# Kernel tuning notes

Measured on AMD Instinct MI355X. Metric: run time of the kernel, lower is better.

## Reference

```python
import jax, jax.numpy as jnp
import numpy as np

B, T, D, H = 8, 512, 1024, 16
DH = D // H  # per-head feature dim (64)


def setup_inputs() -> dict:
    key = jax.random.key(0)
    ks = jax.random.split(key, 10)
    s = 1.0 / np.sqrt(DH)
    inp = {
        "X_data": jax.random.normal(ks[0], (B, T, D), dtype=jnp.float32),
        "mask": jnp.ones((B, T), dtype=jnp.int32),
        # per-head Q/K/V projections (each SelfAttention has its own d_h x d_h weights)
        "Wq": jax.random.normal(ks[1], (H, DH, DH), dtype=jnp.float32) * s,
        "bq": jnp.zeros((H, DH), dtype=jnp.float32),
        "Wk": jax.random.normal(ks[2], (H, DH, DH), dtype=jnp.float32) * s,
        "bk": jnp.zeros((H, DH), dtype=jnp.float32),
        "Wv": jax.random.normal(ks[3], (H, DH, DH), dtype=jnp.float32) * s,
        "bv": jnp.zeros((H, DH), dtype=jnp.float32),
        # AttentionFusion: linear on concatenated head outputs -> len_feature_new
        "Wf": jax.random.normal(ks[4], (D, D), dtype=jnp.float32) * (1.0 / np.sqrt(D)),
        "bf": jnp.zeros((D,), dtype=jnp.float32),
    }
    return inp


def reference(X_data, mask, Wq, bq, Wk, bk, Wv, bv, Wf, bf):
    # Split features into heads: [B, T, H, DH] (equal partitions since D % H == 0)
    Xh = X_data.reshape(B, T, H, DH)
    # Batched per-head projections (replaces the Python loop over heads)
    Q = jnp.einsum("bthd,hde->bhte", Xh, Wq) + bq[None, :, None, :]
    K = jnp.einsum("bthd,hde->bhte", Xh, Wk) + bk[None, :, None, :]
    V = jnp.einsum("bthd,hde->bhte", Xh, Wv) + bv[None, :, None, :]
    scale = 1.0 / jnp.sqrt(jnp.asarray(DH, dtype=Q.dtype))
    scores = jnp.einsum("bhqe,bhke->bhqk", Q, K) * scale  # [B, H, T, T]
    scores = jnp.where(mask[:, None, None, :] > 0, scores, jnp.asarray(-1e9, scores.dtype))
    att = jax.nn.softmax(scores, axis=-1)
    out = jnp.einsum("bhqk,bhke->bhqe", att, V)  # [B, H, T, DH]
    # Concatenate heads (same order as the per-head loop) and fuse
    out = out.transpose(0, 2, 1, 3).reshape(B, T, D)
    fused = out @ Wf + bf  # AttentionFusion linear
    return fused
```

## Files before the change

kernel.cpp:

```cpp
#include <hip/hip_runtime.h>
#include <math.h>

#define B 8
#define T 512
#define D 1024
#define H 16
#define DH 64

typedef __bf16 bf16;
typedef __attribute__((ext_vector_type(8))) __bf16 bf16x8;
typedef __attribute__((ext_vector_type(4))) float f32x4;

__device__ __forceinline__ void gld16(const void* g, void* l) {
    __builtin_amdgcn_global_load_lds(
        (const __attribute__((address_space(1))) void*)g,
        (__attribute__((address_space(3))) void*)l, 16, 0, 0);
}


#define EXP2SCALE 1.44269504088896f

__global__ __launch_bounds__(256) void prep_w(
    const float* __restrict__ Wq, const float* __restrict__ Wk,
    const float* __restrict__ Wv, const float* __restrict__ Wf,
    bf16* __restrict__ WqT, bf16* __restrict__ WkT,
    bf16* __restrict__ WvT, bf16* __restrict__ WfT)
{
    __shared__ bf16 Ts[64 * 72];
    const int blk = blockIdx.x, tid = threadIdx.x;
    if (blk < 48) {
        const int m = blk >> 4, h = blk & 15;
        const float* src = (m == 0 ? Wq : (m == 1 ? Wk : Wv)) + h * 4096;
        bf16* dst = (m == 0 ? WqT : (m == 1 ? WkT : WvT)) + h * 4096;
        for (int i = tid; i < 1024; i += 256) {
            const int d = i >> 4, eq = (i & 15) * 4;
            const float4 w = *(const float4*)(src + d * 64 + eq);
            Ts[(eq + 0) * 72 + d] = (bf16)w.x; Ts[(eq + 1) * 72 + d] = (bf16)w.y;
            Ts[(eq + 2) * 72 + d] = (bf16)w.z; Ts[(eq + 3) * 72 + d] = (bf16)w.w;
        }
        __syncthreads();
        for (int i = tid; i < 512; i += 256) {
            const int e = i >> 3, kc = (i & 7) * 8;
            *(bf16x8*)(dst + e * 64 + kc) = *(const bf16x8*)&Ts[e * 72 + kc];
        }
    } else {
        const int ti = blk - 48, k0 = (ti >> 4) * 64, n0 = (ti & 15) * 64;
        for (int i = tid; i < 1024; i += 256) {
            const int k = i >> 4, nq = (i & 15) * 4;
            const float4 w = *(const float4*)(Wf + (size_t)(k0 + k) * D + n0 + nq);
            Ts[(nq + 0) * 72 + k] = (bf16)w.x; Ts[(nq + 1) * 72 + k] = (bf16)w.y;
            Ts[(nq + 2) * 72 + k] = (bf16)w.z; Ts[(nq + 3) * 72 + k] = (bf16)w.w;
        }
        __syncthreads();
        for (int i = tid; i < 512; i += 256) {
            const int n = i >> 3, kc = (i & 7) * 8;
            *(bf16x8*)(WfT + (size_t)(n0 + n) * D + k0 + kc) = *(const bf16x8*)&Ts[n * 72 + kc];
        }
    }
}

__global__ __launch_bounds__(256, 2) void qkv_attn(
    const float* __restrict__ X, const int* __restrict__ mask,
    const bf16* __restrict__ WqT, const bf16* __restrict__ WkT,
    const bf16* __restrict__ WvT,
    const float* __restrict__ bq, const float* __restrict__ bk,
    const float* __restrict__ bv,
    bf16* __restrict__ Ob)
{
    __shared__ __align__(16) char smem[80384];
    bf16* Wks = (bf16*)(smem);
    bf16* Wvs = (bf16*)(smem + 8192);
    bf16* Pl  = (bf16*)(smem + 53248);
    bf16* Xkt = (bf16*)(smem + 71680);
    int*  msk = (int*)(smem + 79872);
    bf16* Wqs   = (bf16*)(smem + 16384);
    bf16* Xq    = Pl;
    bf16* Stage = Pl;
    bf16* Ostage = Pl;

    const int bh = blockIdx.x & 127, q0 = (blockIdx.x >> 7) * 128;
    const int b = bh >> 4, h = bh & 15;
    const int tid = threadIdx.x, wave = tid >> 6, lane = tid & 63;
    const int quad = lane >> 4, l15 = lane & 15;
    const int lr = lane >> 3, lc = lane & 7;
    const int csw = (lc ^ lr) * 8;

    const int pkrow = wave * 16 + (lane >> 2);
    const int pc0 = (lane & 3) * 2;

    float bqr[4], bkr[4], bvr[4];
#pragma unroll
    for (int nt = 0; nt < 4; ++nt) {
        bqr[nt] = bq[h * DH + nt * 16 + l15];
        bkr[nt] = bk[h * DH + nt * 16 + l15];
        bvr[nt] = bv[h * DH + nt * 16 + l15];
    }

    float4 px0, px1, px2, px3;
    {
        const float* src = X + (size_t)(b * T + pkrow) * D + h * DH + pc0 * 8;
        px0 = *(const float4*)src; px1 = *(const float4*)(src + 4);
        px2 = *(const float4*)(src + 8); px3 = *(const float4*)(src + 12);
    }
    int mreg = (tid < 64) ? mask[(size_t)b * T + tid] : 0;

    {
        const int r1 = wave * 16;
#pragma unroll
        for (int j = 0; j < 2; ++j) {
            gld16(WqT + (size_t)h * 4096 + (r1 + j * 8 + lr) * 64 + csw, &Wqs[(r1 + j * 8) * 64]);
            gld16(WkT + (size_t)h * 4096 + (r1 + j * 8 + lr) * 64 + csw, &Wks[(r1 + j * 8) * 64]);
            gld16(WvT + (size_t)h * 4096 + (r1 + j * 8 + lr) * 64 + csw, &Wvs[(r1 + j * 8) * 64]);
        }
    }
    for (int i = tid; i < 1024; i += 256) {
        const int row = i >> 3, c = i & 7;
        const float* src = X + (size_t)(b * T + q0 + row) * D + h * DH + c * 8;
        const float4 x0 = *(const float4*)src;
        const float4 x1 = *(const float4*)(src + 4);
        bf16x8 t;
        t[0] = (bf16)x0.x; t[1] = (bf16)x0.y; t[2] = (bf16)x0.z; t[3] = (bf16)x0.w;
        t[4] = (bf16)x1.x; t[5] = (bf16)x1.y; t[6] = (bf16)x1.z; t[7] = (bf16)x1.w;
        *(bf16x8*)&Xq[row * 64 + ((c ^ (row & 7)) * 8)] = t;
    }
    __syncthreads();

    {
        f32x4 accQ[2][4] = {};
#pragma unroll
        for (int ks = 0; ks < 2; ++ks) {
            bf16x8 af[2], bfr[4];
#pragma unroll
            for (int mt = 0; mt < 2; ++mt) {
                const int row = wave * 32 + mt * 16 + l15;
                af[mt] = *(const bf16x8*)&Xq[row * 64 + (((ks * 4 + quad) ^ (l15 & 7)) * 8)];
            }
#pragma unroll
            for (int nt = 0; nt < 4; ++nt)
                bfr[nt] = *(const bf16x8*)&Wqs[(nt * 16 + l15) * 64 + (((ks * 4 + quad) ^ (l15 & 7)) * 8)];
#pragma unroll
            for (int mt = 0; mt < 2; ++mt)
#pragma unroll
                for (int nt = 0; nt < 4; ++nt)
                    accQ[mt][nt] = __builtin_amdgcn_mfma_f32_16x16x32_bf16(af[mt], bfr[nt], accQ[mt][nt], 0, 0, 0);
        }
        __syncthreads();
        const float qs = 0.125f * EXP2SCALE;
#pragma unroll
        for (int mt = 0; mt < 2; ++mt)
#pragma unroll
            for (int nt = 0; nt < 4; ++nt)
#pragma unroll
                for (int reg = 0; reg < 4; ++reg)
                    Stage[(wave * 32 + mt * 16 + quad * 4 + reg) * 72 + nt * 16 + l15] =
                        (bf16)((accQ[mt][nt][reg] + bqr[nt]) * qs);
        __builtin_amdgcn_wave_barrier();
    }
    bf16x8 qf[2][2];
#pragma unroll
    for (int mt = 0; mt < 2; ++mt)
#pragma unroll
        for (int ks = 0; ks < 2; ++ks)
            qf[mt][ks] = *(const bf16x8*)&Stage[(wave * 32 + mt * 16 + l15) * 72 + ks * 32 + quad * 8];

    f32x4 acc[2][4] = {};
    float lst[2][4] = {};

    for (int kt = 0; kt < 8; ++kt) {
        const int p = kt & 1;
        bf16* Ks  = (bf16*)(smem + 16384 + p * 9216);
        bf16* Vts = (bf16*)(smem + 34816 + p * 9216);

        {
            bf16x8 t0, t1;
            t0[0] = (bf16)px0.x; t0[1] = (bf16)px0.y; t0[2] = (bf16)px0.z; t0[3] = (bf16)px0.w;
            t0[4] = (bf16)px1.x; t0[5] = (bf16)px1.y; t0[6] = (bf16)px1.z; t0[7] = (bf16)px1.w;
            t1[0] = (bf16)px2.x; t1[1] = (bf16)px2.y; t1[2] = (bf16)px2.z; t1[3] = (bf16)px2.w;
            t1[4] = (bf16)px3.x; t1[5] = (bf16)px3.y; t1[6] = (bf16)px3.z; t1[7] = (bf16)px3.w;
            *(bf16x8*)&Xkt[pkrow * 64 + ((pc0 ^ (pkrow & 7)) * 8)] = t0;
            *(bf16x8*)&Xkt[pkrow * 64 + (((pc0 + 1) ^ (pkrow & 7)) * 8)] = t1;
            if (tid < 64) msk[p * 64 + tid] = mreg;
        }
        __builtin_amdgcn_wave_barrier();

        if (kt < 7) {
            const float* src = X + (size_t)(b * T + (kt + 1) * 64 + pkrow) * D + h * DH + pc0 * 8;
            px0 = *(const float4*)src; px1 = *(const float4*)(src + 4);
            px2 = *(const float4*)(src + 8); px3 = *(const float4*)(src + 12);
            if (tid < 64) mreg = mask[(size_t)b * T + (kt + 1) * 64 + tid];
        }

        {
            bf16x8 afkv[2];
#pragma unroll
            for (int ks = 0; ks < 2; ++ks)
                afkv[ks] = *(const bf16x8*)&Xkt[(wave * 16 + l15) * 64 + (((ks * 4 + quad) ^ (l15 & 7)) * 8)];
            f32x4 accK[4] = {}, accV[4] = {};
#pragma unroll
            for (int ks = 0; ks < 2; ++ks)
#pragma unroll
                for (int nt = 0; nt < 4; ++nt) {
                    const bf16x8 bk8 = *(const bf16x8*)&Wks[(nt * 16 + l15) * 64 + (((ks * 4 + quad) ^ (l15 & 7)) * 8)];
                    accK[nt] = __builtin_amdgcn_mfma_f32_16x16x32_bf16(afkv[ks], bk8, accK[nt], 0, 0, 0);
                    const bf16x8 bv8 = *(const bf16x8*)&Wvs[(nt * 16 + l15) * 64 + (((ks * 4 + quad) ^ (l15 & 7)) * 8)];
                    accV[nt] = __builtin_amdgcn_mfma_f32_16x16x32_bf16(afkv[ks], bv8, accV[nt], 0, 0, 0);
                }
#pragma unroll
            for (int nt = 0; nt < 4; ++nt)
#pragma unroll
                for (int reg = 0; reg < 4; ++reg) {
                    const int key = wave * 16 + quad * 4 + reg;
                    const int e = nt * 16 + l15;
                    Ks[key * 72 + e] = (bf16)(accK[nt][reg] + bkr[nt]);
                    Vts[e * 72 + key] = (bf16)(accV[nt][reg] + bvr[nt]);
                }
        }
        __syncthreads();

        bf16* Plw = Pl + wave * (32 * 72);
        {
            bf16x8 kf[4][2];
#pragma unroll
            for (int nt = 0; nt < 4; ++nt)
#pragma unroll
                for (int ks = 0; ks < 2; ++ks)
                    kf[nt][ks] = *(const bf16x8*)&Ks[(nt * 16 + l15) * 72 + ks * 32 + quad * 8];
            int mv[4];
#pragma unroll
            for (int nt = 0; nt < 4; ++nt) mv[nt] = msk[p * 64 + nt * 16 + l15];
#pragma unroll
            for (int mt = 0; mt < 2; ++mt) {
                f32x4 s[4] = {};
#pragma unroll
                for (int ks = 0; ks < 2; ++ks)
#pragma unroll
                    for (int nt = 0; nt < 4; ++nt)
                        s[nt] = __builtin_amdgcn_mfma_f32_16x16x32_bf16(qf[mt][ks], kf[nt][ks], s[nt], 0, 0, 0);
#pragma unroll
                for (int nt = 0; nt < 4; ++nt)
#pragma unroll
                    for (int reg = 0; reg < 4; ++reg) {
                        const float pv = (mv[nt] > 0) ? exp2f(s[nt][reg]) : 0.f;
                        lst[mt][reg] += pv;
                        Plw[(mt * 16 + quad * 4 + reg) * 72 + nt * 16 + l15] = (bf16)pv;
                    }
            }
        }
        __builtin_amdgcn_wave_barrier();

#pragma unroll
        for (int kc = 0; kc < 2; ++kc) {
            const bf16x8 pf0 = *(const bf16x8*)&Plw[(l15) * 72 + kc * 32 + quad * 8];
            const bf16x8 pf1 = *(const bf16x8*)&Plw[(16 + l15) * 72 + kc * 32 + quad * 8];
#pragma unroll
            for (int nt = 0; nt < 4; ++nt) {
                const bf16x8 vf = *(const bf16x8*)&Vts[(nt * 16 + l15) * 72 + kc * 32 + quad * 8];
                acc[0][nt] = __builtin_amdgcn_mfma_f32_16x16x32_bf16(pf0, vf, acc[0][nt], 0, 0, 0);
                acc[1][nt] = __builtin_amdgcn_mfma_f32_16x16x32_bf16(pf1, vf, acc[1][nt], 0, 0, 0);
            }
        }
    }

    __builtin_amdgcn_wave_barrier();
#pragma unroll
    for (int mt = 0; mt < 2; ++mt)
#pragma unroll
        for (int reg = 0; reg < 4; ++reg) {
            float l = lst[mt][reg];
            l += __shfl_xor(l, 1);
            l += __shfl_xor(l, 2);
            l += __shfl_xor(l, 4);
            l += __shfl_xor(l, 8);
            const float inv = 1.f / l;
            const int row = wave * 32 + mt * 16 + quad * 4 + reg;
#pragma unroll
            for (int nt = 0; nt < 4; ++nt)
                Ostage[row * 72 + nt * 16 + l15] = (bf16)(acc[mt][nt][reg] * inv);
        }
    __syncthreads();
    for (int i = tid; i < 1024; i += 256) {
        const int row = i >> 3, c = (i & 7) * 8;
        *(bf16x8*)(Ob + ((size_t)b * T + q0 + row) * D + h * DH + c) =
            *(const bf16x8*)&Ostage[row * 72 + c];
    }
}

__global__ __launch_bounds__(256, 2) void fuse_mfma(
    const bf16* __restrict__ Ob, const bf16* __restrict__ WfT,
    const float* __restrict__ bfv, float* __restrict__ out)
{
    __shared__ __align__(16) char smem[49152];

    const int col0 = blockIdx.x * 64;
    const int row0 = blockIdx.y * 128;
    const int tid = threadIdx.x, wave = tid >> 6, lane = tid & 63;
    const int quad = lane >> 4, l15 = lane & 15;
    const int lr = lane >> 3, lc = lane & 7;
    const int wm = wave * 32;

    f32x4 acc[2][4] = {};

    auto stage = [&](int k0, int buf) {
        bf16* As = (bf16*)(smem + buf * 16384);
        bf16* Bs = (bf16*)(smem + 32768 + buf * 8192);
#pragma unroll
        for (int j = 0; j < 4; ++j) {
            const int row = wm + j * 8 + lr;
            gld16(Ob + (size_t)(row0 + row) * D + k0 + ((lc ^ (row & 7)) * 8),
                  &As[(wm + j * 8) * 64]);
        }
#pragma unroll
        for (int j = 0; j < 2; ++j) {
            const int row = wave * 16 + j * 8 + lr;
            gld16(WfT + (size_t)(col0 + row) * D + k0 + ((lc ^ (row & 7)) * 8),
                  &Bs[(wave * 16 + j * 8) * 64]);
        }
    };

    stage(0, 0);
    __syncthreads();

    for (int i = 0; i < 16; ++i) {
        const int buf = i & 1;
        if (i < 15) stage((i + 1) * 64, buf ^ 1);
        bf16* As = (bf16*)(smem + buf * 16384);
        bf16* Bs = (bf16*)(smem + 32768 + buf * 8192);
#pragma unroll
        for (int ks = 0; ks < 2; ++ks) {
            bf16x8 af[2], bfr[4];
#pragma unroll
            for (int mt = 0; mt < 2; ++mt) {
                const int row = wm + mt * 16 + l15;
                af[mt] = *(const bf16x8*)&As[row * 64 + (((ks * 4 + quad) ^ (l15 & 7)) * 8)];
            }
#pragma unroll
            for (int nt = 0; nt < 4; ++nt)
                bfr[nt] = *(const bf16x8*)&Bs[(nt * 16 + l15) * 64 + (((ks * 4 + quad) ^ (l15 & 7)) * 8)];
#pragma unroll
            for (int mt = 0; mt < 2; ++mt)
#pragma unroll
                for (int nt = 0; nt < 4; ++nt)
                    acc[mt][nt] = __builtin_amdgcn_mfma_f32_16x16x32_bf16(af[mt], bfr[nt], acc[mt][nt], 0, 0, 0);
        }
        __syncthreads();
    }

    float* Ofs = (float*)smem;
    float bias[4];
#pragma unroll
    for (int nt = 0; nt < 4; ++nt) bias[nt] = bfv[col0 + nt * 16 + l15];
#pragma unroll
    for (int mt = 0; mt < 2; ++mt)
#pragma unroll
        for (int reg = 0; reg < 4; ++reg) {
            const int row = wm + mt * 16 + quad * 4 + reg;
#pragma unroll
            for (int nt = 0; nt < 4; ++nt)
                Ofs[row * 68 + nt * 16 + l15] = acc[mt][nt][reg] + bias[nt];
        }
    __syncthreads();
    for (int i = tid; i < 2048; i += 256) {
        const int row = i >> 4, c = (i & 15) * 4;
        *(float4*)(out + (size_t)(row0 + row) * D + col0 + c) = *(const float4*)&Ofs[row * 68 + c];
    }
}

extern "C" void kernel_launch(void* const* d_in, const int* in_sizes, int n_in,
                              void* d_out, int out_size, void* d_ws, size_t ws_size,
                              hipStream_t stream) {
    const float* X   = (const float*)d_in[0];
    const int* mask  = (const int*)d_in[1];
    const float* Wq  = (const float*)d_in[2];
    const float* bq  = (const float*)d_in[3];
    const float* Wk  = (const float*)d_in[4];
    const float* bk  = (const float*)d_in[5];
    const float* Wv  = (const float*)d_in[6];
    const float* bv  = (const float*)d_in[7];
    const float* Wf  = (const float*)d_in[8];
    const float* bfv = (const float*)d_in[9];
    float* out = (float*)d_out;

    bf16* wsb = (bf16*)d_ws;
    const size_t QN = (size_t)B * H * T * DH;
    bf16* Ob  = wsb;
    bf16* WfT = wsb + QN;
    bf16* WqT = WfT + (size_t)D * D;
    bf16* WkT = WqT + H * DH * DH;
    bf16* WvT = WkT + H * DH * DH;

    prep_w<<<dim3(304), 256, 0, stream>>>(Wq, Wk, Wv, Wf, WqT, WkT, WvT, WfT);
    qkv_attn<<<dim3(512), 256, 0, stream>>>(X, mask, WqT, WkT, WvT, bq, bk, bv, Ob);
    fuse_mfma<<<dim3(D / 64, (B * T) / 128), 256, 0, stream>>>(Ob, WfT, bfv, out);
}
```

Before: 130.7 us.

## Transpose MFMA operands for packed stores, fold biases, widen fusion GEMM tile

Measured after the change: 128.4 us. No clear change (-1.8%).

```diff
diff --git a/kernel.cpp b/kernel.cpp
--- a/kernel.cpp
+++ b/kernel.cpp
@@ -9,6 +9,7 @@
 
 typedef __bf16 bf16;
 typedef __attribute__((ext_vector_type(8))) __bf16 bf16x8;
+typedef __attribute__((ext_vector_type(4))) __bf16 bf16x4;
 typedef __attribute__((ext_vector_type(4))) float f32x4;
 
 __device__ __forceinline__ void gld16(const void* g, void* l) {
@@ -84,15 +85,15 @@
     const int quad = lane >> 4, l15 = lane & 15;
     const int lr = lane >> 3, lc = lane & 7;
     const int csw = (lc ^ lr) * 8;
+    (void)bk;
 
     const int pkrow = wave * 16 + (lane >> 2);
     const int pc0 = (lane & 3) * 2;
 
-    float bqr[4], bkr[4], bvr[4];
+    float bqr[4], bvr[4];
 #pragma unroll
     for (int nt = 0; nt < 4; ++nt) {
         bqr[nt] = bq[h * DH + nt * 16 + l15];
-        bkr[nt] = bk[h * DH + nt * 16 + l15];
         bvr[nt] = bv[h * DH + nt * 16 + l15];
     }
 
@@ -164,7 +165,7 @@
             qf[mt][ks] = *(const bf16x8*)&Stage[(wave * 32 + mt * 16 + l15) * 72 + ks * 32 + quad * 8];
 
     f32x4 acc[2][4] = {};
-    float lst[2][4] = {};
+    float lst2[2] = {0.f, 0.f};
 
     for (int kt = 0; kt < 8; ++kt) {
         const int p = kt & 1;
@@ -201,19 +202,21 @@
 #pragma unroll
                 for (int nt = 0; nt < 4; ++nt) {
                     const bf16x8 bk8 = *(const bf16x8*)&Wks[(nt * 16 + l15) * 64 + (((ks * 4 + quad) ^ (l15 & 7)) * 8)];
-                    accK[nt] = __builtin_amdgcn_mfma_f32_16x16x32_bf16(afkv[ks], bk8, accK[nt], 0, 0, 0);
+                    accK[nt] = __builtin_amdgcn_mfma_f32_16x16x32_bf16(bk8, afkv[ks], accK[nt], 0, 0, 0);
                     const bf16x8 bv8 = *(const bf16x8*)&Wvs[(nt * 16 + l15) * 64 + (((ks * 4 + quad) ^ (l15 & 7)) * 8)];
                     accV[nt] = __builtin_amdgcn_mfma_f32_16x16x32_bf16(afkv[ks], bv8, accV[nt], 0, 0, 0);
                 }
 #pragma unroll
-            for (int nt = 0; nt < 4; ++nt)
-#pragma unroll
-                for (int reg = 0; reg < 4; ++reg) {
-                    const int key = wave * 16 + quad * 4 + reg;
-                    const int e = nt * 16 + l15;
-                    Ks[key * 72 + e] = (bf16)(accK[nt][reg] + bkr[nt]);
-                    Vts[e * 72 + key] = (bf16)(accV[nt][reg] + bvr[nt]);
-                }
+            for (int nt = 0; nt < 4; ++nt) {
+                bf16x4 kp;
+#pragma unroll
+                for (int reg = 0; reg < 4; ++reg) kp[reg] = (bf16)accK[nt][reg];
+                *(bf16x4*)&Ks[(wave * 16 + l15) * 72 + nt * 16 + quad * 4] = kp;
+                bf16x4 vp;
+#pragma unroll
+                for (int reg = 0; reg < 4; ++reg) vp[reg] = (bf16)accV[nt][reg];
+                *(bf16x4*)&Vts[(nt * 16 + l15) * 72 + wave * 16 + quad * 4] = vp;
+            }
         }
         __syncthreads();
 
@@ -225,9 +228,10 @@
 #pragma unroll
                 for (int ks = 0; ks < 2; ++ks)
                     kf[nt][ks] = *(const bf16x8*)&Ks[(nt * 16 + l15) * 72 + ks * 32 + quad * 8];
-            int mv[4];
-#pragma unroll
-            for (int nt = 0; nt < 4; ++nt) mv[nt] = msk[p * 64 + nt * 16 + l15];
+            int4 mv4[4];
+#pragma unroll
+            for (int nt = 0; nt < 4; ++nt)
+                mv4[nt] = *(const int4*)&msk[p * 64 + nt * 16 + quad * 4];
 #pragma unroll
             for (int mt = 0; mt < 2; ++mt) {
                 f32x4 s[4] = {};
@@ -235,15 +239,18 @@
                 for (int ks = 0; ks < 2; ++ks)
 #pragma unroll
                     for (int nt = 0; nt < 4; ++nt)
-                        s[nt] = __builtin_amdgcn_mfma_f32_16x16x32_bf16(qf[mt][ks], kf[nt][ks], s[nt], 0, 0, 0);
-#pragma unroll
-                for (int nt = 0; nt < 4; ++nt)
-#pragma unroll
-                    for (int reg = 0; reg < 4; ++reg) {
-                        const float pv = (mv[nt] > 0) ? exp2f(s[nt][reg]) : 0.f;
-                        lst[mt][reg] += pv;
-                        Plw[(mt * 16 + quad * 4 + reg) * 72 + nt * 16 + l15] = (bf16)pv;
-                    }
+                        s[nt] = __builtin_amdgcn_mfma_f32_16x16x32_bf16(kf[nt][ks], qf[mt][ks], s[nt], 0, 0, 0);
+#pragma unroll
+                for (int nt = 0; nt < 4; ++nt) {
+                    bf16x4 pp;
+                    const float p0 = (mv4[nt].x > 0) ? exp2f(s[nt][0]) : 0.f;
+                    const float p1 = (mv4[nt].y > 0) ? exp2f(s[nt][1]) : 0.f;
+                    const float p2 = (mv4[nt].z > 0) ? exp2f(s[nt][2]) : 0.f;
+                    const float p3 = (mv4[nt].w > 0) ? exp2f(s[nt][3]) : 0.f;
+                    lst2[mt] += (p0 + p1) + (p2 + p3);
+                    pp[0] = (bf16)p0; pp[1] = (bf16)p1; pp[2] = (bf16)p2; pp[3] = (bf16)p3;
+                    *(bf16x4*)&Plw[(mt * 16 + l15) * 72 + nt * 16 + quad * 4] = pp;
+                }
             }
         }
         __builtin_amdgcn_wave_barrier();
@@ -262,20 +269,26 @@
     }
 
     __builtin_amdgcn_wave_barrier();
+    float inv_r[2][4];
+#pragma unroll
+    for (int mt = 0; mt < 2; ++mt) {
+        float l = lst2[mt];
+        l += __shfl_xor(l, 16);
+        l += __shfl_xor(l, 32);
+        const float inv = 1.f / l;
+#pragma unroll
+        for (int reg = 0; reg < 4; ++reg)
+            inv_r[mt][reg] = __shfl(inv, (lane & 48) | (quad * 4 + reg));
+    }
 #pragma unroll
     for (int mt = 0; mt < 2; ++mt)
 #pragma unroll
         for (int reg = 0; reg < 4; ++reg) {
-            float l = lst[mt][reg];
-            l += __shfl_xor(l, 1);
-            l += __shfl_xor(l, 2);
-            l += __shfl_xor(l, 4);
-            l += __shfl_xor(l, 8);
-            const float inv = 1.f / l;
             const int row = wave * 32 + mt * 16 + quad * 4 + reg;
 #pragma unroll
             for (int nt = 0; nt < 4; ++nt)
-                Ostage[row * 72 + nt * 16 + l15] = (bf16)(acc[mt][nt][reg] * inv);
+                Ostage[row * 72 + nt * 16 + l15] =
+                    (bf16)(acc[mt][nt][reg] * inv_r[mt][reg] + bvr[nt]);
         }
     __syncthreads();
     for (int i = tid; i < 1024; i += 256) {
@@ -289,31 +302,27 @@
     const bf16* __restrict__ Ob, const bf16* __restrict__ WfT,
     const float* __restrict__ bfv, float* __restrict__ out)
 {
-    __shared__ __align__(16) char smem[49152];
-
-    const int col0 = blockIdx.x * 64;
+    __shared__ __align__(16) char smem[65536];
+
+    const int col0 = blockIdx.x * 128;
     const int row0 = blockIdx.y * 128;
     const int tid = threadIdx.x, wave = tid >> 6, lane = tid & 63;
     const int quad = lane >> 4, l15 = lane & 15;
     const int lr = lane >> 3, lc = lane & 7;
     const int wm = wave * 32;
 
-    f32x4 acc[2][4] = {};
+    f32x4 acc[2][8] = {};
 
     auto stage = [&](int k0, int buf) {
         bf16* As = (bf16*)(smem + buf * 16384);
-        bf16* Bs = (bf16*)(smem + 32768 + buf * 8192);
+        bf16* Bs = (bf16*)(smem + 32768 + buf * 16384);
 #pragma unroll
         for (int j = 0; j < 4; ++j) {
             const int row = wm + j * 8 + lr;
             gld16(Ob + (size_t)(row0 + row) * D + k0 + ((lc ^ (row & 7)) * 8),
                   &As[(wm + j * 8) * 64]);
-        }
-#pragma unroll
-        for (int j = 0; j < 2; ++j) {
-            const int row = wave * 16 + j * 8 + lr;
             gld16(WfT + (size_t)(col0 + row) * D + k0 + ((lc ^ (row & 7)) * 8),
-                  &Bs[(wave * 16 + j * 8) * 64]);
+                  &Bs[(wm + j * 8) * 64]);
         }
     };
 
@@ -324,44 +333,49 @@
         const int buf = i & 1;
         if (i < 15) stage((i + 1) * 64, buf ^ 1);
         bf16* As = (bf16*)(smem + buf * 16384);
-        bf16* Bs = (bf16*)(smem + 32768 + buf * 8192);
+        bf16* Bs = (bf16*)(smem + 32768 + buf * 16384);
 #pragma unroll
         for (int ks = 0; ks < 2; ++ks) {
-            bf16x8 af[2], bfr[4];
+            bf16x8 af[2], bfr[8];
 #pragma unroll
             for (int mt = 0; mt < 2; ++mt) {
                 const int row = wm + mt * 16 + l15;
                 af[mt] = *(const bf16x8*)&As[row * 64 + (((ks * 4 + quad) ^ (l15 & 7)) * 8)];
             }
 #pragma unroll
-            for (int nt = 0; nt < 4; ++nt)
+            for (int nt = 0; nt < 8; ++nt)
                 bfr[nt] = *(const bf16x8*)&Bs[(nt * 16 + l15) * 64 + (((ks * 4 + quad) ^ (l15 & 7)) * 8)];
 #pragma unroll
             for (int mt = 0; mt < 2; ++mt)
 #pragma unroll
-                for (int nt = 0; nt < 4; ++nt)
+                for (int nt = 0; nt < 8; ++nt)
                     acc[mt][nt] = __builtin_amdgcn_mfma_f32_16x16x32_bf16(af[mt], bfr[nt], acc[mt][nt], 0, 0, 0);
         }
         __syncthreads();
     }
 
     float* Ofs = (float*)smem;
-    float bias[4];
-#pragma unroll
-    for (int nt = 0; nt < 4; ++nt) bias[nt] = bfv[col0 + nt * 16 + l15];
-#pragma unroll
-    for (int mt = 0; mt < 2; ++mt)
-#pragma unroll
-        for (int reg = 0; reg < 4; ++reg) {
-            const int row = wm + mt * 16 + quad * 4 + reg;
-#pragma unroll
-            for (int nt = 0; nt < 4; ++nt)
-                Ofs[row * 68 + nt * 16 + l15] = acc[mt][nt][reg] + bias[nt];
-        }
-    __syncthreads();
-    for (int i = tid; i < 2048; i += 256) {
-        const int row = i >> 4, c = (i & 15) * 4;
-        *(float4*)(out + (size_t)(row0 + row) * D + col0 + c) = *(const float4*)&Ofs[row * 68 + c];
+    float bias[8];
+#pragma unroll
+    for (int nt = 0; nt < 8; ++nt) bias[nt] = bfv[col0 + nt * 16 + l15];
+#pragma unroll
+    for (int cp = 0; cp < 2; ++cp) {
+        if (cp) __syncthreads();
+#pragma unroll
+        for (int mt = 0; mt < 2; ++mt)
+#pragma unroll
+            for (int reg = 0; reg < 4; ++reg) {
+                const int row = wm + mt * 16 + quad * 4 + reg;
+#pragma unroll
+                for (int nn = 0; nn < 4; ++nn)
+                    Ofs[row * 68 + nn * 16 + l15] = acc[mt][cp * 4 + nn][reg] + bias[cp * 4 + nn];
+            }
+        __syncthreads();
+        for (int i = tid; i < 2048; i += 256) {
+            const int row = i >> 4, c = (i & 15) * 4;
+            *(float4*)(out + (size_t)(row0 + row) * D + col0 + cp * 64 + c) =
+                *(const float4*)&Ofs[row * 68 + c];
+        }
     }
 }
 
@@ -390,5 +404,5 @@
 
     prep_w<<<dim3(304), 256, 0, stream>>>(Wq, Wk, Wv, Wf, WqT, WkT, WvT, WfT);
     qkv_attn<<<dim3(512), 256, 0, stream>>>(X, mask, WqT, WkT, WvT, bq, bk, bv, Ob);
-    fuse_mfma<<<dim3(D / 64, (B * T) / 128), 256, 0, stream>>>(Ob, WfT, bfv, out);
+    fuse_mfma<<<dim3(D / 128, (B * T) / 128), 256, 0, stream>>>(Ob, WfT, bfv, out);
 }
```
